# Optimization experiments

Measured on AMD Instinct MI355X. Metric: run time of the kernel, lower is better.

## Reference

```python
import jax, jax.numpy as jnp
import numpy as np
import math

B, N, DEG, D, L = 256, 256, 8, 128, 3  # graphs, nodes/graph, avg degree, feature dim, pool layers


def setup_inputs() -> dict:
    key = jax.random.key(0)
    ks = jax.random.split(key, 12)
    Nn = B * N
    E = B * N * DEG
    x = jax.random.normal(ks[0], (Nn, D), jnp.float32)
    # edges strictly within each graph; graphs laid out contiguously (graph b owns nodes [b*N, (b+1)*N))
    offs = jnp.repeat(jnp.arange(B, dtype=jnp.int32) * N, N * DEG)
    src = offs + jax.random.randint(ks[1], (E,), 0, N, dtype=jnp.int32)
    dst = offs + jax.random.randint(ks[2], (E,), 0, N, dtype=jnp.int32)
    edge_index = jnp.stack([src, dst])
    graph_indices = jnp.repeat(jnp.arange(B, dtype=jnp.int32), N)
    s = 1.0 / math.sqrt(D)
    def w(k, shape):
        return jax.random.normal(k, shape, jnp.float32) * s
    return {
        "x": x,
        "edge_index": edge_index,
        "graph_indices": graph_indices,
        "num_graphs": B,
        "Wq": w(ks[3], (L, D, D)), "bq": jnp.zeros((L, D), jnp.float32),
        "Wk": w(ks[4], (L, D, D)), "bk": jnp.zeros((L, D), jnp.float32),
        "Wv": w(ks[5], (L, D, D)), "bv": jnp.zeros((L, D), jnp.float32),
        "Wskip": w(ks[6], (L, D, D)), "bskip": jnp.zeros((L, D), jnp.float32),
        "Wt": w(ks[7], (L, D, D)), "bt": jnp.zeros((L, D), jnp.float32),
        "gamma": jnp.ones((L, D), jnp.float32) + 0.1 * jax.random.normal(ks[8], (L, D), jnp.float32),
        "beta": 0.1 * jax.random.normal(ks[9], (L, D), jnp.float32),
        "pool_w": w(ks[10], (L, D)),
    }


def reference(x, edge_index, graph_indices, num_graphs, Wq, bq, Wk, bk, Wv, bv,
              Wskip, bskip, Wt, bt, gamma, beta, pool_w):
    Bg = int(num_graphs)
    Nn, d = x.shape
    n = Nn // Bg                       # nodes per graph (equal-size graphs)
    src, dst = edge_index[0], edge_index[1]
    mask = jnp.ones(src.shape, bool)   # edge validity mask (shapes stay static across layers)
    NEG = jnp.float32(-1e30)
    inv_sqrt_d = 1.0 / jnp.sqrt(jnp.float32(d))
    feats = []
    for i in range(Wq.shape[0]):
        Nn_cur = x.shape[0]
        # --- TransformerConv (heads=1, concat, root_weight=True, no edge_dim, eval: no dropout) ---
        q = x @ Wq[i] + bq[i]
        k = x @ Wk[i] + bk[i]
        v = x @ Wv[i] + bv[i]
        logits = jnp.einsum('ed,ed->e', q[dst], k[src]) * inv_sqrt_d   # [E]
        logits = jnp.where(mask, logits, NEG)
        m = jax.ops.segment_max(logits, dst, num_segments=Nn_cur)
        m = jnp.where(m > NEG / 2, m, 0.0)                             # guard empty segments
        ex = jnp.where(mask, jnp.exp(logits - m[dst]), 0.0)
        denom = jax.ops.segment_sum(ex, dst, num_segments=Nn_cur)
        alpha = ex / jnp.maximum(denom[dst], 1e-16)                    # scatter-softmax over incoming edges
        agg = jax.ops.segment_sum(alpha[:, None] * v[src], dst, num_segments=Nn_cur)
        x = agg + (x @ Wskip[i] + bskip[i])
        # --- Linear + ReLU ---
        x = jax.nn.relu(x @ Wt[i] + bt[i])
        # --- BatchNorm1d (training-mode batch stats, eps=1e-5) ---
        mu = x.mean(0)
        var = x.var(0)
        x = (x - mu) / jnp.sqrt(var + 1e-5) * gamma[i] + beta[i]
        # --- TopKPooling(ratio=0.5, nonlinearity=tanh) ---
        w_ = pool_w[i]
        score = jnp.tanh((x @ w_) / jnp.linalg.norm(w_))               # [Nn_cur]
        kk = n // 2
        _, idx = jax.lax.top_k(score.reshape(Bg, n), kk)               # [B, kk] per-graph top-k
        perm = (jnp.arange(Bg, dtype=idx.dtype)[:, None] * n + idx).reshape(-1)
        x = x[perm] * score[perm][:, None]
        # re-index edges; drop edges touching removed nodes via mask
        newid = jnp.full((Nn_cur,), -1, dtype=src.dtype).at[perm].set(
            jnp.arange(Bg * kk, dtype=src.dtype))
        s2, d2 = newid[src], newid[dst]
        mask = mask & (s2 >= 0) & (d2 >= 0)
        src = jnp.where(mask, s2, 0)
        dst = jnp.where(mask, d2, 0)
        n = kk
        # --- readout: gmp | gap | gsp per graph ---
        xr = x.reshape(Bg, n, d)
        feats.append(jnp.concatenate([xr.max(1), xr.mean(1), xr.sum(1)], axis=-1))
    return jnp.concatenate(feats, axis=-1)   # [B, L*3*d]
```

## Files before the change

kernel.cpp:

```cpp
#include <hip/hip_runtime.h>
#include <hip/hip_bf16.h>
#include <math.h>

#define DD     128
#define NGRAPH 256
#define ECAPG  2048
#define ETOT   (NGRAPH*ECAPG)
#define NMAX   65536

typedef __attribute__((ext_vector_type(8))) short bf16x8;
typedef __attribute__((ext_vector_type(4))) float f32x4;

__device__ inline unsigned short rne_bf16(float x){
  union { float f; unsigned u; } c; c.f = x;
  unsigned u = c.u;
  return (unsigned short)((u + 0x7FFFu + ((u>>16)&1u)) >> 16);
}
__device__ inline float bf16f(unsigned short h){
  union { unsigned u; float f; } c; c.u = ((unsigned)h)<<16; return c.f;
}

__device__ inline void gload_lds16(const void* g, void* l){
  __builtin_amdgcn_global_load_lds(
      (const __attribute__((address_space(1))) unsigned*)g,
      (__attribute__((address_space(3))) unsigned*)l, 16, 0, 0);
}

__global__ __launch_bounds__(128) void k_wnorm(const float* pw, float* wni){
  int l = blockIdx.x, t = threadIdx.x;
  __shared__ float s[128];
  float v = pw[l*DD + t];
  s[t] = v*v; __syncthreads();
  for (int o=64;o>0;o>>=1){ if (t<o) s[t]+=s[t+o]; __syncthreads(); }
  if (t==0) wni[l] = 1.0f/sqrtf(s[0]);
}

__global__ __launch_bounds__(128) void k_wprep(const float* Wq, const float* Wk, const float* Wv,
                                               const float* Ws, const float* Wt,
                                               unsigned short* whi, unsigned short* wlo){
  int b = blockIdx.x;
  int w = b>>7, krow = b&127, n = threadIdx.x;
  int layer = w/5, which = w - layer*5;
  const float* W = (which==0)?Wq:(which==1)?Wk:(which==2)?Wv:(which==3)?Ws:Wt;
  float v = W[(size_t)layer*DD*DD + krow*DD + n];
  unsigned short h = rne_bf16(v);
  unsigned short l = rne_bf16(v - bf16f(h));
  whi[(size_t)w*DD*DD + (size_t)n*DD + krow] = h;
  wlo[(size_t)w*DD*DD + (size_t)n*DD + krow] = l;
}

__global__ __launch_bounds__(256) void k_xsplit(const float* __restrict__ X,
                                                unsigned short* __restrict__ xh,
                                                unsigned short* __restrict__ xl, int total4){
  int i = blockIdx.x*256 + threadIdx.x;
  if (i >= total4) return;
  float4 v = ((const float4*)X)[i];
  unsigned short h0=rne_bf16(v.x), h1=rne_bf16(v.y), h2=rne_bf16(v.z), h3=rne_bf16(v.w);
  unsigned short l0=rne_bf16(v.x-bf16f(h0)), l1=rne_bf16(v.y-bf16f(h1)),
                 l2=rne_bf16(v.z-bf16f(h2)), l3=rne_bf16(v.w-bf16f(h3));
  uint2 uh, ul;
  uh.x = (unsigned)h0 | ((unsigned)h1<<16); uh.y = (unsigned)h2 | ((unsigned)h3<<16);
  ul.x = (unsigned)l0 | ((unsigned)l1<<16); ul.y = (unsigned)l2 | ((unsigned)l3<<16);
  ((uint2*)xh)[i] = uh; ((uint2*)xl)[i] = ul;
}

__global__ __launch_bounds__(256) void k_csr(const int* __restrict__ src, const int* __restrict__ dst,
                                             int n, int* row_start, int* row_end, int* ssrc){
  int g = blockIdx.x, t = threadIdx.x;
  const int E = ECAPG;
  int base = g*ECAPG;
  __shared__ int lsrc[ECAPG];
  __shared__ unsigned char ldst8[ECAPG];
  __shared__ unsigned char slotc[ECAPG];
  __shared__ unsigned short off[64][256];
  __shared__ int sc[256];
  __shared__ int rstart[256];
  for (int i=t; i<64*256/2; i+=256) ((unsigned*)off)[i] = 0;
  for (int i=t; i<E; i+=256){ lsrc[i]=src[base+i]; ldst8[i]=(unsigned char)(dst[base+i]-g*n); }
  __syncthreads();
  if (t < 64){
    int e0=t*32;
    for (int i=e0;i<e0+32;i++){ int d=ldst8[i]; slotc[i]=(unsigned char)off[t][d]; off[t][d]++; }
  }
  __syncthreads();
  int tot=0;
  if (t<n){
    for (int c=0;c<64;c++){ int tmp=off[c][t]; off[c][t]=(unsigned short)tot; tot+=tmp; }
  }
  sc[t] = (t<n)?tot:0;
  __syncthreads();
  for (int o=1;o<256;o<<=1){ int add=(t>=o)?sc[t-o]:0; __syncthreads(); sc[t]+=add; __syncthreads(); }
  if (t<n){
    int rs = sc[t]-tot;
    rstart[t]=rs;
    row_start[g*n+t]=base+rs; row_end[g*n+t]=base+rs+tot;
  }
  __syncthreads();
  if (t<64){
    int e0=t*32;
    for (int i=e0;i<e0+32;i++){
      int d=ldst8[i];
      ssrc[base + rstart[d] + off[t][d] + slotc[i]] = lsrc[i];
    }
  }
}

struct GArgs {
  const unsigned short* whi[4];
  const unsigned short* wlo[4];
  const float* bias[4];
  float*       O[4];
};

template<int BN>
__global__ __launch_bounds__(256) void k_gemm_mfma(const unsigned short* __restrict__ XHg,
                                                   const unsigned short* __restrict__ XLg,
                                                   GArgs a, float* __restrict__ psum,
                                                   float* __restrict__ psq){
  __shared__ unsigned short XH[128][32], XL[128][32], WHs[128][32], WLs[128][32];
  int head = BN ? 0 : blockIdx.y;
  const unsigned short* WH = a.whi[head];
  const unsigned short* WL = a.wlo[head];
  size_t rowBase = (size_t)blockIdx.x*128;
  int t = threadIdx.x;
  int w = t>>6, l = t&63;
  int wr = (w>>1)*64, wc = (w&1)*64;
  int lr = l&15, lk = (l>>4)*8;
  f32x4 acc[4][4] = {};
  char* bXH = (char*)&XH[0][0];
  char* bXL = (char*)&XL[0][0];
  char* bWH = (char*)&WHs[0][0];
  char* bWL = (char*)&WLs[0][0];
  for (int kc=0; kc<128; kc+=32){
    __syncthreads();
    #pragma unroll
    for (int s2=0; s2<2; s2++){
      int j  = (w*2+s2)*64 + l;
      int r  = j>>2, g = j&3;
      int gc = (g ^ ((r>>1)&3))*8;
      size_t segOff = (size_t)(w*2+s2)*1024;
      size_t gx = (rowBase + r)*DD + kc + gc;
      size_t gw = (size_t)r*DD + kc + gc;
      gload_lds16(XHg + gx, bXH + segOff);
      gload_lds16(XLg + gx, bXL + segOff);
      gload_lds16(WH  + gw, bWH + segOff);
      gload_lds16(WL  + gw, bWL + segOff);
    }
    __syncthreads();
    bf16x8 ah[4], al[4], bh[4], bl[4];
    #pragma unroll
    for (int m=0;m<4;m++){
      int rr = wr + m*16 + lr;
      int bo = rr*64 + ((lk*2) ^ (((rr>>1)&3)<<4));
      ah[m] = *(const bf16x8*)(bXH + bo);
      al[m] = *(const bf16x8*)(bXL + bo);
    }
    #pragma unroll
    for (int n=0;n<4;n++){
      int rr = wc + n*16 + lr;
      int bo = rr*64 + ((lk*2) ^ (((rr>>1)&3)<<4));
      bh[n] = *(const bf16x8*)(bWH + bo);
      bl[n] = *(const bf16x8*)(bWL + bo);
    }
    #pragma unroll
    for (int m=0;m<4;m++){
      #pragma unroll
      for (int n=0;n<4;n++){
        acc[m][n] = __builtin_amdgcn_mfma_f32_16x16x32_bf16(ah[m], bh[n], acc[m][n], 0,0,0);
        acc[m][n] = __builtin_amdgcn_mfma_f32_16x16x32_bf16(ah[m], bl[n], acc[m][n], 0,0,0);
        acc[m][n] = __builtin_amdgcn_mfma_f32_16x16x32_bf16(al[m], bh[n], acc[m][n], 0,0,0);
      }
    }
  }
  float* O = a.O[head];
  const float* bias = a.bias[head];
  float cs[4] = {0.f,0.f,0.f,0.f}, cq[4] = {0.f,0.f,0.f,0.f};
  #pragma unroll
  for (int n=0;n<4;n++){
    int col = wc + n*16 + lr;
    float bv = bias[col];
    #pragma unroll
    for (int m=0;m<4;m++){
      int rb = wr + m*16 + (l>>4)*4;
      #pragma unroll
      for (int r=0;r<4;r++){
        float o = acc[m][n][r] + bv;
        if (BN) o = fmaxf(o, 0.f);
        O[(rowBase + rb + r)*DD + col] = o;
        if (BN){ cs[n] += o; cq[n] += o*o; }
      }
    }
  }
  if (BN){
    __syncthreads();
    float* redS = (float*)&XH[0][0];
    float* redQ = (float*)&XL[0][0];
    int rg = w*4 + (l>>4);
    #pragma unroll
    for (int n=0;n<4;n++){
      int col = wc + n*16 + lr;
      redS[rg*128 + col] = cs[n];
      redQ[rg*128 + col] = cq[n];
    }
    __syncthreads();
    if (t < 128){
      int c = t, w0 = (c>=64) ? 1 : 0;
      float s = 0.f, s2 = 0.f;
      #pragma unroll
      for (int dw=0; dw<2; dw++){
        int ww = w0 + dw*2;
        #pragma unroll
        for (int lq=0; lq<4; lq++){
          s  += redS[(ww*4+lq)*128 + c];
          s2 += redQ[(ww*4+lq)*128 + c];
        }
      }
      psum[blockIdx.x*DD + c] = s;
      psq [blockIdx.x*DD + c] = s2;
    }
  }
}

__global__ __launch_bounds__(256) void k_attn_par(
    const float* __restrict__ q, const float* __restrict__ k, const float* __restrict__ v,
    const int* __restrict__ row_start, const int* __restrict__ row_end,
    const int* __restrict__ ssrc, const float* __restrict__ skip,
    unsigned short* __restrict__ xh, unsigned short* __restrict__ xl)
{
  __shared__ float lg[4][128];
  int nb8 = gridDim.x >> 3;
  int p = blockIdx.x;
  int lb = (p&7)*nb8 + (p>>3);
  int w = threadIdx.x>>6, l = threadIdx.x&63;
  int node = lb*4 + w;
  size_t nb = (size_t)node*DD;
  int s0 = row_start[node], deg = row_end[node]-s0; if (deg>128) deg=128;
  int h8 = l>>3, gl = l&7;
  float4 qv0 = *(const float4*)(q + nb + gl*16);
  float4 qv1 = *(const float4*)(q + nb + gl*16 + 4);
  float4 qv2 = *(const float4*)(q + nb + gl*16 + 8);
  float4 qv3 = *(const float4*)(q + nb + gl*16 + 12);
  const float isd = 0.088388347648318447f;
  for (int base=0; base<deg; base+=8){
    int e = base + h8;
    int s = ssrc[s0 + (e<deg ? e : 0)];
    const float* kp = k + (size_t)s*DD + gl*16;
    float4 k0=*(const float4*)kp, k1=*(const float4*)(kp+4),
           k2=*(const float4*)(kp+8), k3=*(const float4*)(kp+12);
    float pd = qv0.x*k0.x+qv0.y*k0.y+qv0.z*k0.z+qv0.w*k0.w
             + qv1.x*k1.x+qv1.y*k1.y+qv1.z*k1.z+qv1.w*k1.w
             + qv2.x*k2.x+qv2.y*k2.y+qv2.z*k2.z+qv2.w*k2.w
             + qv3.x*k3.x+qv3.y*k3.y+qv3.z*k3.z+qv3.w*k3.w;
    pd += __shfl_xor(pd,1,64); pd += __shfl_xor(pd,2,64); pd += __shfl_xor(pd,4,64);
    if (gl==0 && e<deg) lg[w][e] = pd*isd;
  }
  float v1 = (l    <deg) ? lg[w][l]    : -1e30f;
  float v2 = (64+l <deg) ? lg[w][64+l] : -1e30f;
  float m = fmaxf(v1,v2);
  #pragma unroll
  for (int o=32;o>0;o>>=1) m = fmaxf(m, __shfl_xor(m,o,64));
  float e1 = (l   <deg) ? __expf(v1-m) : 0.f;
  float e2 = (64+l<deg) ? __expf(v2-m) : 0.f;
  float dn = e1+e2;
  #pragma unroll
  for (int o=32;o>0;o>>=1) dn += __shfl_xor(dn,o,64);
  float rd = 1.0f/fmaxf(dn, 1e-16f);
  if (l   <deg) lg[w][l]    = e1*rd;
  if (64+l<deg) lg[w][64+l] = e2*rd;
  int degp = (deg+7)&~7;
  if (l < degp-deg) lg[w][deg+l] = 0.f;
  float a0=0.f, a1=0.f;
  for (int base=0; base<degp; base+=8){
    int ss[8];
    #pragma unroll
    for (int e=0;e<8;e++){
      int idx = base+e;
      ss[e] = ssrc[s0 + (idx<deg ? idx : deg-1)];
    }
    float2 vv[8];
    #pragma unroll
    for (int e=0;e<8;e++) vv[e] = *(const float2*)(v + (size_t)ss[e]*DD + l*2);
    #pragma unroll
    for (int e=0;e<8;e++){
      float al = lg[w][base+e];
      a0 += al*vv[e].x; a1 += al*vv[e].y;
    }
  }
  float2 sk = *(const float2*)(skip + nb + l*2);
  float x0 = sk.x + a0, x1 = sk.y + a1;
  unsigned short h0=rne_bf16(x0), h1=rne_bf16(x1);
  unsigned short l0=rne_bf16(x0-bf16f(h0)), l1=rne_bf16(x1-bf16f(h1));
  *(unsigned*)(xh + nb + l*2) = (unsigned)h0 | ((unsigned)h1<<16);
  *(unsigned*)(xl + nb + l*2) = (unsigned)l0 | ((unsigned)l1<<16);
}

__global__ __launch_bounds__(256) void k_bnfin(const float* __restrict__ psum,
                                               const float* __restrict__ psq,
                                               float* mu, float* istd, float invN, int nblk){
  int c = blockIdx.x, t = threadIdx.x;
  __shared__ float sh[256], sh2[256];
  float s=0.f, s2=0.f;
  for (int b=t; b<nblk; b+=256){ s += psum[b*DD+c]; s2 += psq[b*DD+c]; }
  sh[t]=s; sh2[t]=s2; __syncthreads();
  for (int o=128;o>0;o>>=1){
    if (t<o){ sh[t]+=sh[t+o]; sh2[t]+=sh2[t+o]; }
    __syncthreads();
  }
  if (t==0){
    float m = sh[0]*invN;
    float var = fmaxf(sh2[0]*invN - m*m, 0.f);
    mu[c]=m; istd[c] = 1.0f/sqrtf(var + 1e-5f);
  }
}

__global__ __launch_bounds__(256) void k_pool(
    const float* __restrict__ h, const float* __restrict__ mu, const float* __restrict__ istd,
    const float* __restrict__ gma, const float* __restrict__ bta,
    const float* __restrict__ pw, const float* __restrict__ wni, int layer, int n,
    const int* __restrict__ osrc, const int* __restrict__ odst, const int* __restrict__ oecnt,
    unsigned short* __restrict__ xh, unsigned short* __restrict__ xl,
    float* __restrict__ out,
    int* __restrict__ nsrc, int* __restrict__ ndst, int* __restrict__ necnt,
    int* __restrict__ row_start, int* __restrict__ row_end, int* __restrict__ ssrc, int do_edges)
{
  int g = blockIdx.x, t = threadIdx.x;
  int kk = n>>1;
  __shared__ float bnp[5][128];
  __shared__ float ss[256];
  __shared__ int   sel[128];
  __shared__ float skp[128];
  __shared__ int   nid[256];
  __shared__ float redm[4][128], rdsum[4][128];
  __shared__ int   esrc[ECAPG], edst[ECAPG];
  __shared__ int   sc[256];
  __shared__ unsigned short off2[64][128];
  __shared__ unsigned char  slot2[ECAPG];
  __shared__ int   rstart2[128];

  if (t<128){ bnp[0][t]=mu[t]; bnp[1][t]=istd[t]; bnp[2][t]=gma[t]; bnp[3][t]=bta[t]; bnp[4][t]=pw[t]; }
  __syncthreads();
  if (t<n){
    const float* hr = h + ((size_t)g*n + t)*DD;
    float dot = 0.f;
    for (int c=0;c<DD;c+=4){
      float4 hv = *(const float4*)(hr+c);
      dot += ((hv.x-bnp[0][c+0])*bnp[1][c+0]*bnp[2][c+0]+bnp[3][c+0])*bnp[4][c+0];
      dot += ((hv.y-bnp[0][c+1])*bnp[1][c+1]*bnp[2][c+1]+bnp[3][c+1])*bnp[4][c+1];
      dot += ((hv.z-bnp[0][c+2])*bnp[1][c+2]*bnp[2][c+2]+bnp[3][c+2])*bnp[4][c+2];
      dot += ((hv.w-bnp[0][c+3])*bnp[1][c+3]*bnp[2][c+3]+bnp[3][c+3])*bnp[4][c+3];
    }
    ss[t] = tanhf(dot * wni[0]);
  }
  __syncthreads();
  if (t<n){
    float si = ss[t]; int rank = 0;
    for (int j=0;j<n;j++){ float sj = ss[j]; rank += (sj>si)||((sj==si)&&(j<t)); }
    if (rank<kk){ sel[rank]=t; skp[rank]=si; nid[t]=rank; } else nid[t]=-1;
  }
  __syncthreads();
  int w = t>>6, l = t&63, d0 = l*2;
  float m0=-1e30f, m1=-1e30f, sm0=0.f, sm1=0.f;
  for (int p=w; p<kk; p+=4){
    int srow = sel[p]; float scv = skp[p];
    float2 hv = *(const float2*)(h + ((size_t)g*n + srow)*DD + d0);
    float x0 = ((hv.x-bnp[0][d0  ])*bnp[1][d0  ]*bnp[2][d0  ]+bnp[3][d0  ])*scv;
    float x1 = ((hv.y-bnp[0][d0+1])*bnp[1][d0+1]*bnp[2][d0+1]+bnp[3][d0+1])*scv;
    m0 = fmaxf(m0,x0); m1 = fmaxf(m1,x1); sm0 += x0; sm1 += x1;
    unsigned short h0=rne_bf16(x0), h1=rne_bf16(x1);
    unsigned short l0=rne_bf16(x0-bf16f(h0)), l1=rne_bf16(x1-bf16f(h1));
    size_t ob = ((size_t)g*kk + p)*DD + d0;
    *(unsigned*)(xh+ob) = (unsigned)h0 | ((unsigned)h1<<16);
    *(unsigned*)(xl+ob) = (unsigned)l0 | ((unsigned)l1<<16);
  }
  redm[w][d0]=m0; redm[w][d0+1]=m1; rdsum[w][d0]=sm0; rdsum[w][d0+1]=sm1;
  __syncthreads();
  if (t<128){
    float mx = fmaxf(fmaxf(redm[0][t],redm[1][t]), fmaxf(redm[2][t],redm[3][t]));
    float sm = rdsum[0][t]+rdsum[1][t]+rdsum[2][t]+rdsum[3][t];
    float* ob = out + (size_t)g*1152 + layer*384;
    ob[t]=mx; ob[128+t]=sm/(float)kk; ob[256+t]=sm;
  }
  if (!do_edges) return;
  int E = oecnt ? oecnt[g] : ECAPG;
  int base = g*ECAPG;
  int cl = 0;
  for (int j=0;j<8;j++){ int i=t*8+j;
    if (i<E){ int ns=nid[osrc[base+i]-g*n], nd=nid[odst[base+i]-g*n]; if ((ns|nd)>=0) cl++; } }
  sc[t]=cl; __syncthreads();
  for (int o=1;o<256;o<<=1){ int add=(t>=o)?sc[t-o]:0; __syncthreads(); sc[t]+=add; __syncthreads(); }
  int off = sc[t]-cl;
  for (int j=0;j<8;j++){ int i=t*8+j;
    if (i<E){ int ns=nid[osrc[base+i]-g*n], nd=nid[odst[base+i]-g*n];
      if ((ns|nd)>=0){ esrc[off]=ns; edst[off]=nd; off++; } } }
  int Etot = sc[255];
  __syncthreads();
  if (t==0) necnt[g]=Etot;
  for (int i=t;i<Etot;i+=256){ nsrc[base+i]=esrc[i]+g*kk; ndst[base+i]=edst[i]+g*kk; }
  for (int i=t; i<64*128/2; i+=256) ((unsigned*)off2)[i] = 0;
  __syncthreads();
  int nch = (Etot+31)>>5;
  if (t<nch){
    int e0=t*32, e1 = (e0+32<Etot)?(e0+32):Etot;
    for (int i=e0;i<e1;i++){ int d=edst[i]; slot2[i]=(unsigned char)off2[t][d]; off2[t][d]++; }
  }
  __syncthreads();
  int tot=0;
  if (t<kk){
    for (int c=0;c<nch;c++){ int tmp=off2[c][t]; off2[c][t]=(unsigned short)tot; tot+=tmp; }
  }
  sc[t] = (t<kk)?tot:0;
  __syncthreads();
  for (int o=1;o<256;o<<=1){ int add=(t>=o)?sc[t-o]:0; __syncthreads(); sc[t]+=add; __syncthreads(); }
  if (t<kk){
    int rs = sc[t]-tot;
    rstart2[t]=rs;
    row_start[g*kk+t]=base+rs; row_end[g*kk+t]=base+rs+tot;
  }
  __syncthreads();
  if (t<nch){
    int e0=t*32, e1 = (e0+32<Etot)?(e0+32):Etot;
    for (int i=e0;i<e1;i++){
      int d=edst[i];
      ssrc[base + rstart2[d] + off2[t][d] + slot2[i]] = esrc[i] + g*kk;
    }
  }
}

extern "C" void kernel_launch(void* const* d_in, const int* in_sizes, int n_in,
                              void* d_out, int out_size, void* d_ws, size_t ws_size,
                              hipStream_t stream){
  const float* x0   = (const float*)d_in[0];
  const int*   eidx = (const int*)d_in[1];
  const float* Wq = (const float*)d_in[4];  const float* bq = (const float*)d_in[5];
  const float* Wk = (const float*)d_in[6];  const float* bk = (const float*)d_in[7];
  const float* Wv = (const float*)d_in[8];  const float* bv = (const float*)d_in[9];
  const float* Wsk= (const float*)d_in[10]; const float* bsk= (const float*)d_in[11];
  const float* Wt = (const float*)d_in[12]; const float* bt = (const float*)d_in[13];
  const float* gamma = (const float*)d_in[14]; const float* beta = (const float*)d_in[15];
  const float* pw = (const float*)d_in[16];

  char* w8 = (char*)d_ws;
  size_t off = 0;
  auto alloc = [&](size_t bytes)->void*{ void* p = w8+off; off += (bytes+255)&~(size_t)255; return p; };

  float* qb  = (float*)alloc((size_t)NMAX*DD*4);
  float* kb  = (float*)alloc((size_t)NMAX*DD*4);
  float* vb  = (float*)alloc((size_t)NMAX*DD*4);
  float* xsb = (float*)alloc((size_t)NMAX*DD*4);
  unsigned short* xh = (unsigned short*)alloc((size_t)NMAX*DD*2);
  unsigned short* xl = (unsigned short*)alloc((size_t)NMAX*DD*2);
  unsigned short* whi = (unsigned short*)alloc((size_t)15*DD*DD*2);
  unsigned short* wlo = (unsigned short*)alloc((size_t)15*DD*DD*2);
  float* psum = (float*)alloc((size_t)512*DD*4);
  float* psq  = (float*)alloc((size_t)512*DD*4);
  float* mu   = (float*)alloc(DD*4);
  float* istd = (float*)alloc(DD*4);
  float* wni  = (float*)alloc(64);
  int* row_start = (int*)alloc(NMAX*4);
  int* row_end   = (int*)alloc(NMAX*4);
  int* ssrc      = (int*)alloc(ETOT*4);
  int* srcA = (int*)alloc(ETOT*4);
  int* dstA = (int*)alloc(ETOT*4);
  int* srcB = (int*)alloc(ETOT*4);
  int* dstB = (int*)alloc(ETOT*4);
  int* ecntA = (int*)alloc(NGRAPH*4);
  int* ecntB = (int*)alloc(NGRAPH*4);

  k_wnorm<<<3,128,0,stream>>>(pw, wni);
  k_wprep<<<15*128,128,0,stream>>>(Wq, Wk, Wv, Wsk, Wt, whi, wlo);
  k_xsplit<<<NMAX/8,256,0,stream>>>(x0, xh, xl, NMAX*32);
  k_csr<<<NGRAPH,256,0,stream>>>(eidx, eidx+ETOT, 256, row_start, row_end, ssrc);

  const int* csrc = eidx;
  const int* cdst = eidx + ETOT;
  const int* cecnt = nullptr;
  int n = 256;

  for (int layer=0; layer<3; layer++){
    int Nn = NGRAPH * n;
    int kk = n/2;

    GArgs h4;
    h4.whi[0]=whi+(size_t)(layer*5+0)*DD*DD; h4.wlo[0]=wlo+(size_t)(layer*5+0)*DD*DD; h4.bias[0]=bq +layer*DD; h4.O[0]=qb;
    h4.whi[1]=whi+(size_t)(layer*5+1)*DD*DD; h4.wlo[1]=wlo+(size_t)(layer*5+1)*DD*DD; h4.bias[1]=bk +layer*DD; h4.O[1]=kb;
    h4.whi[2]=whi+(size_t)(layer*5+2)*DD*DD; h4.wlo[2]=wlo+(size_t)(layer*5+2)*DD*DD; h4.bias[2]=bv +layer*DD; h4.O[2]=vb;
    h4.whi[3]=whi+(size_t)(layer*5+3)*DD*DD; h4.wlo[3]=wlo+(size_t)(layer*5+3)*DD*DD; h4.bias[3]=bsk+layer*DD; h4.O[3]=xsb;
    k_gemm_mfma<0><<<dim3(Nn/128,4),256,0,stream>>>(xh, xl, h4, nullptr, nullptr);

    k_attn_par<<<Nn/4,256,0,stream>>>(qb, kb, vb, row_start, row_end, ssrc, xsb, xh, xl);

    GArgs h1;
    h1.whi[0]=whi+(size_t)(layer*5+4)*DD*DD; h1.wlo[0]=wlo+(size_t)(layer*5+4)*DD*DD; h1.bias[0]=bt+layer*DD; h1.O[0]=qb;
    h1.whi[1]=h1.whi[0]; h1.wlo[1]=h1.wlo[0]; h1.bias[1]=h1.bias[0]; h1.O[1]=qb;
    h1.whi[2]=h1.whi[0]; h1.wlo[2]=h1.wlo[0]; h1.bias[2]=h1.bias[0]; h1.O[2]=qb;
    h1.whi[3]=h1.whi[0]; h1.wlo[3]=h1.wlo[0]; h1.bias[3]=h1.bias[0]; h1.O[3]=qb;
    k_gemm_mfma<1><<<dim3(Nn/128,1),256,0,stream>>>(xh, xl, h1, psum, psq);

    k_bnfin<<<128,256,0,stream>>>(psum, psq, mu, istd, 1.0f/(float)Nn, Nn/128);

    int* nsrc  = (layer==0) ? srcA : srcB;
    int* ndst  = (layer==0) ? dstA : dstB;
    int* necnt = (layer==0) ? ecntA : ecntB;
    k_pool<<<NGRAPH,256,0,stream>>>(qb, mu, istd, gamma+layer*DD, beta+layer*DD,
                                    pw+layer*DD, wni+layer, layer, n,
                                    csrc, cdst, cecnt, xh, xl, (float*)d_out,
                                    nsrc, ndst, necnt, row_start, row_end, ssrc, layer<2 ? 1 : 0);

    csrc = nsrc; cdst = ndst; cecnt = necnt;
    n = kk;
  }
}
```

Before: 363.6 us.

## Process two nodes per wavefront in attention kernel with cached source indices

The attention kernel now assigns two destination nodes per 64-lane wavefront (32 lanes each), so the grid is halved. Source indices are cached in shared memory during the score pass and reused in the aggregation pass, which now loads float4 V rows one edge at a time instead of batches of 8 float2 loads. Offsets switch to 32-bit unsigned arithmetic. This raises per-lane work and the bytes per load while cutting redundant ssrc reads, but it can lose memory-level parallelism in the serial V loop, and the two half-waves diverge when their degrees differ.

```diff
diff --git a/kernel.cpp b/kernel.cpp
--- a/kernel.cpp
+++ b/kernel.cpp
@@ -227,24 +227,31 @@
     const int* __restrict__ ssrc, const float* __restrict__ skip,
     unsigned short* __restrict__ xh, unsigned short* __restrict__ xl)
 {
-  __shared__ float lg[4][128];
+  __shared__ float lg[4][2][128];
+  __shared__ int   se[4][2][128];
   int nb8 = gridDim.x >> 3;
   int p = blockIdx.x;
   int lb = (p&7)*nb8 + (p>>3);
   int w = threadIdx.x>>6, l = threadIdx.x&63;
-  int node = lb*4 + w;
-  size_t nb = (size_t)node*DD;
-  int s0 = row_start[node], deg = row_end[node]-s0; if (deg>128) deg=128;
-  int h8 = l>>3, gl = l&7;
-  float4 qv0 = *(const float4*)(q + nb + gl*16);
-  float4 qv1 = *(const float4*)(q + nb + gl*16 + 4);
-  float4 qv2 = *(const float4*)(q + nb + gl*16 + 8);
-  float4 qv3 = *(const float4*)(q + nb + gl*16 + 12);
+  int h = l>>5, q32 = l&31;
+  int node = lb*8 + w*2 + h;
+  int s0 = row_start[node];
+  int deg = row_end[node]-s0; if (deg>128) deg=128;
+  int maxd = max(deg, __shfl_xor(deg, 32, 64));
+  int grp = q32>>3, gl = q32&7;
   const float isd = 0.088388347648318447f;
-  for (int base=0; base<deg; base+=8){
-    int e = base + h8;
-    int s = ssrc[s0 + (e<deg ? e : 0)];
-    const float* kp = k + (size_t)s*DD + gl*16;
+  unsigned qoff = ((unsigned)node<<7) + (unsigned)(gl<<4);
+  float4 qv0 = *(const float4*)(q + qoff);
+  float4 qv1 = *(const float4*)(q + qoff + 4);
+  float4 qv2 = *(const float4*)(q + qoff + 8);
+  float4 qv3 = *(const float4*)(q + qoff + 12);
+  if (q32==0) se[w][h][0] = 0;
+  for (int base=0; base<maxd; base+=4){
+    int e = base + grp;
+    int eok = (e<deg);
+    int s = ssrc[s0 + (eok ? e : 0)];
+    unsigned ko = ((unsigned)s<<7) + (unsigned)(gl<<4);
+    const float* kp = k + ko;
     float4 k0=*(const float4*)kp, k1=*(const float4*)(kp+4),
            k2=*(const float4*)(kp+8), k3=*(const float4*)(kp+12);
     float pd = qv0.x*k0.x+qv0.y*k0.y+qv0.z*k0.z+qv0.w*k0.w
@@ -252,46 +259,47 @@
              + qv2.x*k2.x+qv2.y*k2.y+qv2.z*k2.z+qv2.w*k2.w
              + qv3.x*k3.x+qv3.y*k3.y+qv3.z*k3.z+qv3.w*k3.w;
     pd += __shfl_xor(pd,1,64); pd += __shfl_xor(pd,2,64); pd += __shfl_xor(pd,4,64);
-    if (gl==0 && e<deg) lg[w][e] = pd*isd;
-  }
-  float v1 = (l    <deg) ? lg[w][l]    : -1e30f;
-  float v2 = (64+l <deg) ? lg[w][64+l] : -1e30f;
-  float m = fmaxf(v1,v2);
+    if (gl==0 && eok){ lg[w][h][e] = pd*isd; se[w][h][e] = s; }
+  }
+  float x0v = (q32    <deg) ? lg[w][h][q32]    : -1e30f;
+  float x1v = (32+q32 <deg) ? lg[w][h][32+q32] : -1e30f;
+  float x2v = (64+q32 <deg) ? lg[w][h][64+q32] : -1e30f;
+  float x3v = (96+q32 <deg) ? lg[w][h][96+q32] : -1e30f;
+  float m = fmaxf(fmaxf(x0v,x1v), fmaxf(x2v,x3v));
   #pragma unroll
-  for (int o=32;o>0;o>>=1) m = fmaxf(m, __shfl_xor(m,o,64));
-  float e1 = (l   <deg) ? __expf(v1-m) : 0.f;
-  float e2 = (64+l<deg) ? __expf(v2-m) : 0.f;
-  float dn = e1+e2;
+  for (int o=16;o>0;o>>=1) m = fmaxf(m, __shfl_xor(m,o,64));
+  float e0 = (q32   <deg) ? __expf(x0v-m) : 0.f;
+  float e1 = (32+q32<deg) ? __expf(x1v-m) : 0.f;
+  float e2 = (64+q32<deg) ? __expf(x2v-m) : 0.f;
+  float e3 = (96+q32<deg) ? __expf(x3v-m) : 0.f;
+  float dn = (e0+e1)+(e2+e3);
   #pragma unroll
-  for (int o=32;o>0;o>>=1) dn += __shfl_xor(dn,o,64);
+  for (int o=16;o>0;o>>=1) dn += __shfl_xor(dn,o,64);
   float rd = 1.0f/fmaxf(dn, 1e-16f);
-  if (l   <deg) lg[w][l]    = e1*rd;
-  if (64+l<deg) lg[w][64+l] = e2*rd;
-  int degp = (deg+7)&~7;
-  if (l < degp-deg) lg[w][deg+l] = 0.f;
-  float a0=0.f, a1=0.f;
-  for (int base=0; base<degp; base+=8){
-    int ss[8];
-    #pragma unroll
-    for (int e=0;e<8;e++){
-      int idx = base+e;
-      ss[e] = ssrc[s0 + (idx<deg ? idx : deg-1)];
-    }
-    float2 vv[8];
-    #pragma unroll
-    for (int e=0;e<8;e++) vv[e] = *(const float2*)(v + (size_t)ss[e]*DD + l*2);
-    #pragma unroll
-    for (int e=0;e<8;e++){
-      float al = lg[w][base+e];
-      a0 += al*vv[e].x; a1 += al*vv[e].y;
-    }
-  }
-  float2 sk = *(const float2*)(skip + nb + l*2);
-  float x0 = sk.x + a0, x1 = sk.y + a1;
-  unsigned short h0=rne_bf16(x0), h1=rne_bf16(x1);
-  unsigned short l0=rne_bf16(x0-bf16f(h0)), l1=rne_bf16(x1-bf16f(h1));
-  *(unsigned*)(xh + nb + l*2) = (unsigned)h0 | ((unsigned)h1<<16);
-  *(unsigned*)(xl + nb + l*2) = (unsigned)l0 | ((unsigned)l1<<16);
+  if (q32   <deg) lg[w][h][q32]    = e0*rd;
+  if (32+q32<deg) lg[w][h][32+q32] = e1*rd;
+  if (64+q32<deg) lg[w][h][64+q32] = e2*rd;
+  if (96+q32<deg) lg[w][h][96+q32] = e3*rd;
+  float4 a = make_float4(0.f,0.f,0.f,0.f);
+  unsigned dcol = (unsigned)(q32<<2);
+  for (int e=0; e<maxd; e++){
+    int eok = (e<deg);
+    int s  = se[w][h][eok ? e : 0];
+    float al = eok ? lg[w][h][e] : 0.f;
+    float4 vv = *(const float4*)(v + (((unsigned)s<<7) + dcol));
+    a.x += al*vv.x; a.y += al*vv.y; a.z += al*vv.z; a.w += al*vv.w;
+  }
+  unsigned ob = ((unsigned)node<<7) + dcol;
+  float4 sk = *(const float4*)(skip + ob);
+  float x0 = sk.x + a.x, x1 = sk.y + a.y, x2 = sk.z + a.z, x3 = sk.w + a.w;
+  unsigned short h0=rne_bf16(x0), h1=rne_bf16(x1), h2=rne_bf16(x2), h3=rne_bf16(x3);
+  unsigned short lo0=rne_bf16(x0-bf16f(h0)), lo1=rne_bf16(x1-bf16f(h1)),
+                 lo2=rne_bf16(x2-bf16f(h2)), lo3=rne_bf16(x3-bf16f(h3));
+  uint2 uh, ul;
+  uh.x = (unsigned)h0 | ((unsigned)h1<<16); uh.y = (unsigned)h2 | ((unsigned)h3<<16);
+  ul.x = (unsigned)lo0 | ((unsigned)lo1<<16); ul.y = (unsigned)lo2 | ((unsigned)lo3<<16);
+  *(uint2*)(xh + ob) = uh;
+  *(uint2*)(xl + ob) = ul;
 }
 
 __global__ __launch_bounds__(256) void k_bnfin(const float* __restrict__ psum,
@@ -487,7 +495,7 @@
     h4.whi[3]=whi+(size_t)(layer*5+3)*DD*DD; h4.wlo[3]=wlo+(size_t)(layer*5+3)*DD*DD; h4.bias[3]=bsk+layer*DD; h4.O[3]=xsb;
     k_gemm_mfma<0><<<dim3(Nn/128,4),256,0,stream>>>(xh, xl, h4, nullptr, nullptr);
 
-    k_attn_par<<<Nn/4,256,0,stream>>>(qb, kb, vb, row_start, row_end, ssrc, xsb, xh, xl);
+    k_attn_par<<<Nn/8,256,0,stream>>>(qb, kb, vb, row_start, row_end, ssrc, xsb, xh, xl);
 
     GArgs h1;
     h1.whi[0]=whi+(size_t)(layer*5+4)*DD*DD; h1.wlo[0]=wlo+(size_t)(layer*5+4)*DD*DD; h1.bias[0]=bt+layer*DD; h1.O[0]=qb;
```

New measurement: 322.6 us. -11.3%, faster.
